# Performance work log

Hardware: AMD Instinct MI355X
Metric: run time of the kernel (lower is better)

Reference implementation:

```python
import jax, jax.numpy as jnp
import numpy as np

B, S, D = 2, 2048, 1024
H, HD = 16, 64
DFF = 4 * D
EPS = 1e-5


def gelu(x):
    return 0.5 * x * (1.0 + jnp.tanh(jnp.sqrt(2.0 / jnp.pi) * (x + 0.044715 * x * x * x)))


def layer_norm(x, scale, bias):
    mu = jnp.mean(x, axis=-1, keepdims=True)
    var = jnp.mean(jnp.square(x - mu), axis=-1, keepdims=True)
    return (x - mu) * jax.lax.rsqrt(var + EPS) * scale + bias


def setup_inputs() -> dict:
    key = jax.random.key(0)
    ks = jax.random.split(key, 8)
    s = 0.02
    x = jax.random.normal(ks[0], (B, S, D), jnp.float32)
    mask = jnp.tril(jnp.ones((S, S), dtype=bool))[None, None]  # (1,1,S,S) causal
    return {
        "x": x,
        "mask": mask,
        "ln1_scale": jnp.ones((D,), jnp.float32),
        "ln1_bias": jnp.zeros((D,), jnp.float32),
        "ln2_scale": jnp.ones((D,), jnp.float32),
        "ln2_bias": jnp.zeros((D,), jnp.float32),
        "w_qkv": jax.random.normal(ks[1], (D, 3 * D), jnp.float32) * s,
        "b_qkv": jnp.zeros((3 * D,), jnp.float32),
        "w_attn_proj": jax.random.normal(ks[2], (D, D), jnp.float32) * s,
        "b_attn_proj": jnp.zeros((D,), jnp.float32),
        "w_fc": jax.random.normal(ks[3], (D, DFF), jnp.float32) * s,
        "b_fc": jnp.zeros((DFF,), jnp.float32),
        "w_mlp_proj": jax.random.normal(ks[4], (DFF, D), jnp.float32) * s,
        "b_mlp_proj": jnp.zeros((D,), jnp.float32),
    }


def reference(x, mask, ln1_scale, ln1_bias, ln2_scale, ln2_bias,
              w_qkv, b_qkv, w_attn_proj, b_attn_proj,
              w_fc, b_fc, w_mlp_proj, b_mlp_proj):
    bsz, seq, _ = x.shape
    # --- attention branch ---
    h = layer_norm(x, ln1_scale, ln1_bias)
    qkv = h @ w_qkv + b_qkv                       # (b, s, 3D)
    q, k, v = jnp.split(qkv, 3, axis=-1)
    q = q.reshape(bsz, seq, H, HD).transpose(0, 2, 1, 3)  # bhsd
    k = k.reshape(bsz, seq, H, HD).transpose(0, 2, 1, 3)
    v = v.reshape(bsz, seq, H, HD).transpose(0, 2, 1, 3)
    q = q * (1.0 / jnp.sqrt(HD))
    scores = jnp.einsum('bhqd,bhkd->bhqk', q, k)
    scores = jnp.where(mask, scores, -1e10)
    probs = jax.nn.softmax(scores, axis=-1)
    attn = jnp.einsum('bhqk,bhkd->bhqd', probs, v)
    attn = attn.transpose(0, 2, 1, 3).reshape(bsz, seq, D)
    attn = attn @ w_attn_proj + b_attn_proj
    x = x + attn
    # --- MLP branch ---
    h = layer_norm(x, ln2_scale, ln2_bias)
    h = gelu(h @ w_fc + b_fc)
    h = h @ w_mlp_proj + b_mlp_proj
    return x + h
```

## Files before the change

### kernel.cpp

```cpp
#include <hip/hip_runtime.h>
#include <hip/hip_bf16.h>
#include <stdint.h>


typedef __attribute__((ext_vector_type(8))) short bf16x8;
typedef __attribute__((ext_vector_type(8))) unsigned short u16x8;
typedef __attribute__((ext_vector_type(4))) float f32x4;

#define NEG_BIG -30000.0f
#define EXP2SC 0.18033688011112042f

__device__ __forceinline__ float b2f(unsigned short u) {
  union { unsigned int i; float f; } c; c.i = ((unsigned int)u) << 16; return c.f;
}
__device__ __forceinline__ unsigned short f2b(float f) {
  union { float f; unsigned int u; } c; c.f = f;
  unsigned int r = c.u + 0x7fffu + ((c.u >> 16) & 1u);
  return (unsigned short)(r >> 16);
}
__device__ __forceinline__ unsigned int pk2bf(float a, float b) {
  float2 f; f.x = a; f.y = b;
  union { __hip_bfloat162 h; unsigned int u; } c;
  c.h = __float22bfloat162_rn(f);
  return c.u;
}
__device__ __forceinline__ float ldx(const void* p, size_t i, int f32) {
  return f32 ? ((const float*)p)[i] : b2f(((const unsigned short*)p)[i]);
}
__device__ __forceinline__ void gld_lds16(const void* g, void* l) {
  __builtin_amdgcn_global_load_lds(
      (__attribute__((address_space(1))) void*)(void*)g,
      (__attribute__((address_space(3))) void*)l, 16, 0, 0);
}

__global__ void detect_k(const unsigned short* __restrict__ x, int* __restrict__ flag) {
  int lane = threadIdx.x;
  int cnt = 0;
#pragma unroll
  for (int j = 0; j < 4; ++j) {
    unsigned e = (x[lane * 4 + j] >> 7) & 0xFF;
    if (e >= 100 && e <= 145) cnt++;
  }
#pragma unroll
  for (int off = 32; off; off >>= 1) cnt += __shfl_down(cnt, off);
  if (lane == 0) *flag = (cnt < 220) ? 1 : 0;
}

__global__ __launch_bounds__(256) void transpose_k(
    const void* __restrict__ in, unsigned short* __restrict__ out,
    int K, int N, const int* __restrict__ flag) {
  int fm = *flag;
  __shared__ unsigned short tile[64][72];
  int n0 = blockIdx.x * 64, k0 = blockIdx.y * 64;
  int t = threadIdx.x;
  int r = t >> 3, c0 = (t & 7) * 8;
  if (fm) {
    const float* inf = (const float*)in;
#pragma unroll
    for (int p = 0; p < 2; ++p) {
      int k = r + p * 32;
      float4 v0 = *(const float4*)(inf + (size_t)(k0 + k) * N + n0 + c0);
      float4 v1 = *(const float4*)(inf + (size_t)(k0 + k) * N + n0 + c0 + 4);
      tile[k][c0 + 0] = f2b(v0.x); tile[k][c0 + 1] = f2b(v0.y);
      tile[k][c0 + 2] = f2b(v0.z); tile[k][c0 + 3] = f2b(v0.w);
      tile[k][c0 + 4] = f2b(v1.x); tile[k][c0 + 5] = f2b(v1.y);
      tile[k][c0 + 6] = f2b(v1.z); tile[k][c0 + 7] = f2b(v1.w);
    }
  } else {
    const unsigned short* inu = (const unsigned short*)in;
#pragma unroll
    for (int p = 0; p < 2; ++p) {
      int k = r + p * 32;
      u16x8 v = *(const u16x8*)(inu + (size_t)(k0 + k) * N + n0 + c0);
      *(u16x8*)&tile[k][c0] = v;
    }
  }
  __syncthreads();
#pragma unroll
  for (int p = 0; p < 2; ++p) {
    int n = r + p * 32;
    u16x8 v;
#pragma unroll
    for (int j = 0; j < 8; ++j) v[j] = tile[c0 + j][n];
    *(u16x8*)(out + (size_t)(n0 + n) * K + k0 + c0) = v;
  }
}

__global__ __launch_bounds__(256) void ln_k(
    const void* __restrict__ x, const void* __restrict__ sc,
    const void* __restrict__ bs, unsigned short* __restrict__ out,
    const int* __restrict__ flag, int xAdap) {
  int fm = *flag;
  int fx = xAdap ? fm : 0;
  int row = blockIdx.x, t = threadIdx.x;
  float f0, f1, f2, f3;
  if (fx) {
    float4 xv = ((const float4*)x)[(size_t)row * 256 + t];
    f0 = xv.x; f1 = xv.y; f2 = xv.z; f3 = xv.w;
  } else {
    ushort4 xv = ((const ushort4*)x)[(size_t)row * 256 + t];
    f0 = b2f(xv.x); f1 = b2f(xv.y); f2 = b2f(xv.z); f3 = b2f(xv.w);
  }
  float s = f0 + f1 + f2 + f3;
  float q = f0 * f0 + f1 * f1 + f2 * f2 + f3 * f3;
#pragma unroll
  for (int off = 32; off; off >>= 1) {
    s += __shfl_down(s, off);
    q += __shfl_down(q, off);
  }
  __shared__ float red[8];
  int w = t >> 6, lane = t & 63;
  if (lane == 0) { red[w] = s; red[w + 4] = q; }
  __syncthreads();
  float S = red[0] + red[1] + red[2] + red[3];
  float Q = red[4] + red[5] + red[6] + red[7];
  float mean = S * (1.f / 1024.f);
  float var = Q * (1.f / 1024.f) - mean * mean;
  float rstd = rsqrtf(var + 1e-5f);
  int c = t * 4;
  ushort4 o;
  o.x = f2b((f0 - mean) * rstd * ldx(sc, c, fm)     + ldx(bs, c, fm));
  o.y = f2b((f1 - mean) * rstd * ldx(sc, c + 1, fm) + ldx(bs, c + 1, fm));
  o.z = f2b((f2 - mean) * rstd * ldx(sc, c + 2, fm) + ldx(bs, c + 2, fm));
  o.w = f2b((f3 - mean) * rstd * ldx(sc, c + 3, fm) + ldx(bs, c + 3, fm));
  ((ushort4*)(out + (size_t)row * 1024))[t] = o;
}

template <int EPI>
__global__ __launch_bounds__(256) void gemm_bt(
    const unsigned short* __restrict__ A, const unsigned short* __restrict__ Bt,
    const void* __restrict__ bias, const void* __restrict__ res,
    void* __restrict__ C, int M, int N, int K,
    const int* __restrict__ flag, int resAdap, int outAdap) {
  int fm = *flag;
  int fr = resAdap ? fm : 0;
  int fo = outAdap ? fm : 0;
  __shared__ unsigned short As[2][128 * 32];
  __shared__ unsigned short Bs[2][128 * 32];
  int t = threadIdx.x;
  int bn = blockIdx.x * 128, bm = blockIdx.y * 128;
  int w = t >> 6, lane = t & 63, quad = lane >> 4, l16 = lane & 15;
  int wm = (w >> 1) * 64, wn = (w & 1) * 64;
  f32x4 acc[4][4] = {};

  int c1 = t, c2 = t + 256;
  int r1 = c1 >> 2, e1 = (c1 & 3) * 8;
  int r2 = c2 >> 2, e2 = (c2 & 3) * 8;
  const unsigned short* a1 = A + (size_t)(bm + r1) * K + e1;
  const unsigned short* a2 = A + (size_t)(bm + r2) * K + e2;
  const unsigned short* b1 = Bt + (size_t)(bn + r1) * K + e1;
  const unsigned short* b2 = Bt + (size_t)(bn + r2) * K + e2;

  for (int k0 = 0; k0 < K; k0 += 64) {
    gld_lds16(a1 + k0,      As[0] + c1 * 8);
    gld_lds16(a2 + k0,      As[0] + c2 * 8);
    gld_lds16(a1 + k0 + 32, As[1] + c1 * 8);
    gld_lds16(a2 + k0 + 32, As[1] + c2 * 8);
    gld_lds16(b1 + k0,      Bs[0] + c1 * 8);
    gld_lds16(b2 + k0,      Bs[0] + c2 * 8);
    gld_lds16(b1 + k0 + 32, Bs[1] + c1 * 8);
    gld_lds16(b2 + k0 + 32, Bs[1] + c2 * 8);
    __syncthreads();
#pragma unroll
    for (int h = 0; h < 2; ++h) {
      bf16x8 af[4], bfr[4];
#pragma unroll
      for (int i = 0; i < 4; ++i)
        af[i] = *(const bf16x8*)&As[h][(wm + i * 16 + l16) * 32 + quad * 8];
#pragma unroll
      for (int j = 0; j < 4; ++j)
        bfr[j] = *(const bf16x8*)&Bs[h][(wn + j * 16 + l16) * 32 + quad * 8];
#pragma unroll
      for (int i = 0; i < 4; ++i)
#pragma unroll
        for (int j = 0; j < 4; ++j)
          acc[i][j] = __builtin_amdgcn_mfma_f32_16x16x32_bf16(af[i], bfr[j], acc[i][j], 0, 0, 0);
    }
    __syncthreads();
  }

#pragma unroll
  for (int j = 0; j < 4; ++j) {
    int col = bn + wn + j * 16 + l16;
    float bb = ldx(bias, col, fm);
#pragma unroll
    for (int i = 0; i < 4; ++i) {
      int row0 = bm + wm + i * 16 + quad * 4;
#pragma unroll
      for (int r = 0; r < 4; ++r) {
        float v = acc[i][j][r] + bb;
        if (EPI == 1) {
          float u = 0.7978845608f * (v + 0.044715f * v * v * v);
          float e = __expf(2.f * u);
          float th = 1.f - 2.f / (e + 1.f);
          v = 0.5f * v * (1.f + th);
        } else if (EPI == 2) {
          v += ldx(res, (size_t)(row0 + r) * N + col, fr);
        }
        size_t idx = (size_t)(row0 + r) * N + col;
        if (fo) ((float*)C)[idx] = v;
        else    ((unsigned short*)C)[idx] = f2b(v);
      }
    }
  }
}

__global__ __launch_bounds__(256) void gemm_pk(
    const unsigned short* __restrict__ A, const unsigned short* __restrict__ Bt,
    float* __restrict__ P, int M, int N, int Kh, int Kfull) {
  __shared__ unsigned short As[2][128 * 32];
  __shared__ unsigned short Bs[2][128 * 32];
  int t = threadIdx.x;
  int bn = blockIdx.x * 128, bm = blockIdx.y * 128;
  int koff = blockIdx.z * Kh;
  float* Pz = P + (size_t)blockIdx.z * M * N;
  int w = t >> 6, lane = t & 63, quad = lane >> 4, l16 = lane & 15;
  int wm = (w >> 1) * 64, wn = (w & 1) * 64;
  f32x4 acc[4][4] = {};

  int c1 = t, c2 = t + 256;
  int r1 = c1 >> 2, e1 = (c1 & 3) * 8;
  int r2 = c2 >> 2, e2 = (c2 & 3) * 8;
  const unsigned short* a1 = A + (size_t)(bm + r1) * Kfull + koff + e1;
  const unsigned short* a2 = A + (size_t)(bm + r2) * Kfull + koff + e2;
  const unsigned short* b1 = Bt + (size_t)(bn + r1) * Kfull + koff + e1;
  const unsigned short* b2 = Bt + (size_t)(bn + r2) * Kfull + koff + e2;

  for (int k0 = 0; k0 < Kh; k0 += 64) {
    gld_lds16(a1 + k0,      As[0] + c1 * 8);
    gld_lds16(a2 + k0,      As[0] + c2 * 8);
    gld_lds16(a1 + k0 + 32, As[1] + c1 * 8);
    gld_lds16(a2 + k0 + 32, As[1] + c2 * 8);
    gld_lds16(b1 + k0,      Bs[0] + c1 * 8);
    gld_lds16(b2 + k0,      Bs[0] + c2 * 8);
    gld_lds16(b1 + k0 + 32, Bs[1] + c1 * 8);
    gld_lds16(b2 + k0 + 32, Bs[1] + c2 * 8);
    __syncthreads();
#pragma unroll
    for (int h = 0; h < 2; ++h) {
      bf16x8 af[4], bfr[4];
#pragma unroll
      for (int i = 0; i < 4; ++i)
        af[i] = *(const bf16x8*)&As[h][(wm + i * 16 + l16) * 32 + quad * 8];
#pragma unroll
      for (int j = 0; j < 4; ++j)
        bfr[j] = *(const bf16x8*)&Bs[h][(wn + j * 16 + l16) * 32 + quad * 8];
#pragma unroll
      for (int i = 0; i < 4; ++i)
#pragma unroll
        for (int j = 0; j < 4; ++j)
          acc[i][j] = __builtin_amdgcn_mfma_f32_16x16x32_bf16(af[i], bfr[j], acc[i][j], 0, 0, 0);
    }
    __syncthreads();
  }

#pragma unroll
  for (int j = 0; j < 4; ++j) {
    int col = bn + wn + j * 16 + l16;
#pragma unroll
    for (int i = 0; i < 4; ++i) {
      int row0 = bm + wm + i * 16 + quad * 4;
#pragma unroll
      for (int r = 0; r < 4; ++r)
        Pz[(size_t)(row0 + r) * N + col] = acc[i][j][r];
    }
  }
}

__global__ __launch_bounds__(256) void reduce2_k(
    const float* __restrict__ P0, const float* __restrict__ P1,
    const void* __restrict__ bias, const void* __restrict__ res,
    void* __restrict__ out, int N,
    const int* __restrict__ flag, int resAdap, int outAdap) {
  int fm = *flag;
  int fr = resAdap ? fm : 0;
  int fo = outAdap ? fm : 0;
  size_t idx = ((size_t)blockIdx.x * 256 + threadIdx.x) * 4;
  float4 p0 = *(const float4*)(P0 + idx);
  float4 p1 = *(const float4*)(P1 + idx);
  int col = (int)(idx & (size_t)(N - 1));
  float v0 = p0.x + p1.x + ldx(bias, col, fm)     + ldx(res, idx, fr);
  float v1 = p0.y + p1.y + ldx(bias, col + 1, fm) + ldx(res, idx + 1, fr);
  float v2 = p0.z + p1.z + ldx(bias, col + 2, fm) + ldx(res, idx + 2, fr);
  float v3 = p0.w + p1.w + ldx(bias, col + 3, fm) + ldx(res, idx + 3, fr);
  if (fo) {
    float4 o; o.x = v0; o.y = v1; o.z = v2; o.w = v3;
    *(float4*)((float*)out + idx) = o;
  } else {
    ushort4 o; o.x = f2b(v0); o.y = f2b(v1); o.z = f2b(v2); o.w = f2b(v3);
    *(ushort4*)((unsigned short*)out + idx) = o;
  }
}

__global__ __launch_bounds__(256) void attn_k(
    const unsigned short* __restrict__ qkv, unsigned short* __restrict__ out) {
  __shared__ unsigned short Ks[64 * 72];
  __shared__ unsigned int   Vt[64 * 35];
  __shared__ unsigned short Ps[4 * 16 * 72];
  int t = threadIdx.x, w = t >> 6, lane = t & 63, quad = lane >> 4, l16 = lane & 15;
  int pi = blockIdx.x, bh = blockIdx.y, b = bh >> 4, h = bh & 15;
  const unsigned short* base = qkv + (size_t)b * 2048 * 3072 + h * 64;
  unsigned short* Pw = Ps + w * 16 * 72;
  int srow = t >> 3, d0 = (t & 7) * 8;

#pragma unroll 1
  for (int half = 0; half < 2; ++half) {
    int qt = half ? (31 - pi) : pi;
    int q0 = qt * 64;
    int qrel = w * 16 + l16;
    const unsigned short* qp = base + (size_t)(q0 + qrel) * 3072;
    bf16x8 bq0 = *(const bf16x8*)(qp + quad * 8);
    bf16x8 bq1 = *(const bf16x8*)(qp + 32 + quad * 8);
    float m_i = NEG_BIG, l_i = 0.f;
    f32x4 O[4] = {};

    u16x8 kA, kB, vA, vB;
    {
      const unsigned short* kb = base;
      kA = *(const u16x8*)(kb + (size_t)srow * 3072 + 1024 + d0);
      kB = *(const u16x8*)(kb + (size_t)(srow + 32) * 3072 + 1024 + d0);
      vA = *(const u16x8*)(kb + (size_t)(2 * srow) * 3072 + 2048 + d0);
      vB = *(const u16x8*)(kb + (size_t)(2 * srow + 1) * 3072 + 2048 + d0);
    }

#pragma unroll 1
    for (int kt = 0; kt <= qt; ++kt) {
      *(u16x8*)&Ks[srow * 72 + d0] = kA;
      *(u16x8*)&Ks[(srow + 32) * 72 + d0] = kB;
#pragma unroll
      for (int j = 0; j < 8; ++j)
        Vt[(d0 + j) * 35 + srow] = (unsigned int)vA[j] | ((unsigned int)vB[j] << 16);
      __syncthreads();

      if (kt < qt) {
        const unsigned short* kb = base + (size_t)((kt + 1) * 64) * 3072;
        kA = *(const u16x8*)(kb + (size_t)srow * 3072 + 1024 + d0);
        kB = *(const u16x8*)(kb + (size_t)(srow + 32) * 3072 + 1024 + d0);
        vA = *(const u16x8*)(kb + (size_t)(2 * srow) * 3072 + 2048 + d0);
        vB = *(const u16x8*)(kb + (size_t)(2 * srow + 1) * 3072 + 2048 + d0);
      }

      f32x4 ST[4];
#pragma unroll
      for (int i = 0; i < 4; ++i) {
        bf16x8 ak0 = *(const bf16x8*)&Ks[(i * 16 + l16) * 72 + quad * 8];
        bf16x8 ak1 = *(const bf16x8*)&Ks[(i * 16 + l16) * 72 + 32 + quad * 8];
        f32x4 z = {};
        z = __builtin_amdgcn_mfma_f32_16x16x32_bf16(ak0, bq0, z, 0, 0, 0);
        ST[i] = __builtin_amdgcn_mfma_f32_16x16x32_bf16(ak1, bq1, z, 0, 0, 0);
      }

      bool dm = (kt == qt);
      float p[4][4];
      float mx = NEG_BIG;
#pragma unroll
      for (int i = 0; i < 4; ++i)
#pragma unroll
        for (int r = 0; r < 4; ++r) {
          float v = ST[i][r] * EXP2SC;
          int srel = i * 16 + quad * 4 + r;
          if (dm && srel > qrel) v = NEG_BIG;
          p[i][r] = v;
          mx = fmaxf(mx, v);
        }
      mx = fmaxf(mx, __shfl_xor(mx, 16));
      mx = fmaxf(mx, __shfl_xor(mx, 32));
      float mn = fmaxf(m_i, mx);
      float alpha = exp2f(m_i - mn);
      m_i = mn;
      float sum = 0.f;
#pragma unroll
      for (int i = 0; i < 4; ++i)
#pragma unroll
        for (int r = 0; r < 4; ++r) {
          float e = exp2f(p[i][r] - mn);
          p[i][r] = e;
          sum += e;
        }
      sum += __shfl_xor(sum, 16);
      sum += __shfl_xor(sum, 32);
      l_i = alpha * l_i + sum;

#pragma unroll
      for (int i = 0; i < 4; ++i) {
        uint2 pr;
        pr.x = pk2bf(p[i][0], p[i][1]);
        pr.y = pk2bf(p[i][2], p[i][3]);
        *(uint2*)(Pw + l16 * 72 + i * 16 + quad * 4) = pr;
      }

      float ar[4];
#pragma unroll
      for (int r = 0; r < 4; ++r)
        ar[r] = __shfl(alpha, (lane & 48) | (quad * 4 + r));
#pragma unroll
      for (int jd = 0; jd < 4; ++jd)
#pragma unroll
        for (int r = 0; r < 4; ++r) O[jd][r] *= ar[r];

#pragma unroll
      for (int ks = 0; ks < 2; ++ks) {
        bf16x8 ap = *(const bf16x8*)(Pw + l16 * 72 + ks * 32 + quad * 8);
#pragma unroll
        for (int jd = 0; jd < 4; ++jd) {
          union { unsigned int u[4]; bf16x8 v; } bv;
          int vbase = (jd * 16 + l16) * 35 + ks * 16 + quad * 4;
#pragma unroll
          for (int cc = 0; cc < 4; ++cc) bv.u[cc] = Vt[vbase + cc];
          O[jd] = __builtin_amdgcn_mfma_f32_16x16x32_bf16(ap, bv.v, O[jd], 0, 0, 0);
        }
      }
      __syncthreads();
    }

    float li[4];
#pragma unroll
    for (int r = 0; r < 4; ++r)
      li[r] = 1.f / __shfl(l_i, (lane & 48) | (quad * 4 + r));
#pragma unroll
    for (int jd = 0; jd < 4; ++jd)
#pragma unroll
      for (int r = 0; r < 4; ++r) {
        size_t row = (size_t)b * 2048 + q0 + w * 16 + quad * 4 + r;
        out[row * 1024 + h * 64 + jd * 16 + l16] = f2b(O[jd][r] * li[r]);
      }
  }
}

extern "C" void kernel_launch(void* const* d_in, const int* in_sizes, int n_in,
                              void* d_out, int out_size, void* d_ws, size_t ws_size,
                              hipStream_t stream) {
  (void)in_sizes; (void)n_in; (void)out_size;
  const void* x     = d_in[0];
  const void* ln1s  = d_in[2];
  const void* ln1b  = d_in[3];
  const void* ln2s  = d_in[4];
  const void* ln2b  = d_in[5];
  const void* w_qkv = d_in[6];
  const void* b_qkv = d_in[7];
  const void* w_ap  = d_in[8];
  const void* b_ap  = d_in[9];
  const void* w_fc  = d_in[10];
  const void* b_fc  = d_in[11];
  const void* w_mp  = d_in[12];
  const void* b_mp  = d_in[13];
  char* ws = (char*)d_ws;

  const int M = 4096, D = 1024, DFF = 4096, QKV3 = 3072;
  size_t off = 0;
  auto alloc = [&](size_t n) { char* p = ws + off; off += n; return p; };
  int* flag            = (int*)alloc(256);
  unsigned short* wT   = (unsigned short*)alloc((size_t)DFF * D * 2);
  unsigned short* hbuf = (unsigned short*)alloc((size_t)M * D * 2);
  unsigned short* x1   = (unsigned short*)alloc((size_t)M * D * 2);
  char* region = alloc((size_t)M * DFF * 2);
  unsigned short* qkvb = (unsigned short*)region;
  float* P0a = (float*)region;
  float* P1a = (float*)(region + (size_t)M * D * 4);
  unsigned short* fcb  = (unsigned short*)region;
  bool mlpSplit = ws_size >= off + (size_t)M * D * 8 + 1024;
  float* P0m = (float*)(ws + off);
  float* P1m = P0m + (size_t)M * D;

  dim3 blk(256);
  detect_k<<<dim3(1), dim3(64), 0, stream>>>((const unsigned short*)x, flag);
  transpose_k<<<dim3(QKV3 / 64, D / 64), blk, 0, stream>>>(w_qkv, wT, D, QKV3, flag);
  ln_k<<<dim3(M), blk, 0, stream>>>(x, ln1s, ln1b, hbuf, flag, 1);
  gemm_bt<0><<<dim3(QKV3 / 128, M / 128), blk, 0, stream>>>(hbuf, wT, b_qkv, nullptr, qkvb, M, QKV3, D, flag, 0, 0);
  attn_k<<<dim3(16, 32), blk, 0, stream>>>(qkvb, hbuf);
  transpose_k<<<dim3(D / 64, D / 64), blk, 0, stream>>>(w_ap, wT, D, D, flag);
  gemm_pk<<<dim3(D / 128, M / 128, 2), blk, 0, stream>>>(hbuf, wT, P0a, M, D, D / 2, D);
  reduce2_k<<<dim3(M * D / 1024), blk, 0, stream>>>(P0a, P1a, b_ap, x, x1, D, flag, 1, 0);
  transpose_k<<<dim3(DFF / 64, D / 64), blk, 0, stream>>>(w_fc, wT, D, DFF, flag);
  ln_k<<<dim3(M), blk, 0, stream>>>(x1, ln2s, ln2b, hbuf, flag, 0);
  gemm_bt<1><<<dim3(DFF / 128, M / 128), blk, 0, stream>>>(hbuf, wT, b_fc, nullptr, fcb, M, DFF, D, flag, 0, 0);
  transpose_k<<<dim3(D / 64, DFF / 64), blk, 0, stream>>>(w_mp, wT, DFF, D, flag);
  if (mlpSplit) {
    gemm_pk<<<dim3(D / 128, M / 128, 2), blk, 0, stream>>>(fcb, wT, P0m, M, D, DFF / 2, DFF);
    reduce2_k<<<dim3(M * D / 1024), blk, 0, stream>>>(P0m, P1m, b_mp, x1, d_out, D, flag, 0, 1);
  } else {
    gemm_bt<2><<<dim3(D / 128, M / 128), blk, 0, stream>>>(fcb, wT, b_mp, x1, d_out, M, D, DFF, flag, 0, 1);
  }
}
```

Baseline: 417.4 us.

## Replace direct global-to-LDS loads with register-prefetched double-buffered GEMM pipeline

Both GEMM kernels drop the global_load_lds path, which loaded a 64-wide K slab and then synchronised twice per iteration. They now prefetch the next 32-wide K slice into registers while MFMAs run on the current LDS buffer, and alternate between two LDS buffers so only one barrier is needed per iteration. The intent is to hide global memory latency behind compute and remove one barrier per step. In exchange the loop runs twice as many iterations with less work each, uses more registers, and goes through VGPRs instead of the direct DMA-to-LDS path.

```diff
diff --git a/kernel.cpp b/kernel.cpp
--- a/kernel.cpp
+++ b/kernel.cpp
@@ -26,11 +26,6 @@
 }
 __device__ __forceinline__ float ldx(const void* p, size_t i, int f32) {
   return f32 ? ((const float*)p)[i] : b2f(((const unsigned short*)p)[i]);
-}
-__device__ __forceinline__ void gld_lds16(const void* g, void* l) {
-  __builtin_amdgcn_global_load_lds(
-      (__attribute__((address_space(1))) void*)(void*)g,
-      (__attribute__((address_space(3))) void*)l, 16, 0, 0);
 }
 
 __global__ void detect_k(const unsigned short* __restrict__ x, int* __restrict__ flag) {
@@ -151,32 +146,39 @@
   const unsigned short* b1 = Bt + (size_t)(bn + r1) * K + e1;
   const unsigned short* b2 = Bt + (size_t)(bn + r2) * K + e2;
 
-  for (int k0 = 0; k0 < K; k0 += 64) {
-    gld_lds16(a1 + k0,      As[0] + c1 * 8);
-    gld_lds16(a2 + k0,      As[0] + c2 * 8);
-    gld_lds16(a1 + k0 + 32, As[1] + c1 * 8);
-    gld_lds16(a2 + k0 + 32, As[1] + c2 * 8);
-    gld_lds16(b1 + k0,      Bs[0] + c1 * 8);
-    gld_lds16(b2 + k0,      Bs[0] + c2 * 8);
-    gld_lds16(b1 + k0 + 32, Bs[1] + c1 * 8);
-    gld_lds16(b2 + k0 + 32, Bs[1] + c2 * 8);
+  u16x8 va1 = *(const u16x8*)a1;
+  u16x8 va2 = *(const u16x8*)a2;
+  u16x8 vb1 = *(const u16x8*)b1;
+  u16x8 vb2 = *(const u16x8*)b2;
+
+  int nIter = K >> 5;
+  for (int it = 0; it < nIter; ++it) {
+    unsigned short* Ab = As[it & 1];
+    unsigned short* Bb = Bs[it & 1];
+    *(u16x8*)(Ab + c1 * 8) = va1;
+    *(u16x8*)(Ab + c2 * 8) = va2;
+    *(u16x8*)(Bb + c1 * 8) = vb1;
+    *(u16x8*)(Bb + c2 * 8) = vb2;
     __syncthreads();
-#pragma unroll
-    for (int h = 0; h < 2; ++h) {
-      bf16x8 af[4], bfr[4];
-#pragma unroll
-      for (int i = 0; i < 4; ++i)
-        af[i] = *(const bf16x8*)&As[h][(wm + i * 16 + l16) * 32 + quad * 8];
+    if (it + 1 < nIter) {
+      int k0 = (it + 1) << 5;
+      va1 = *(const u16x8*)(a1 + k0);
+      va2 = *(const u16x8*)(a2 + k0);
+      vb1 = *(const u16x8*)(b1 + k0);
+      vb2 = *(const u16x8*)(b2 + k0);
+    }
+    bf16x8 af[4], bfr[4];
+#pragma unroll
+    for (int i = 0; i < 4; ++i)
+      af[i] = *(const bf16x8*)&Ab[(wm + i * 16 + l16) * 32 + quad * 8];
+#pragma unroll
+    for (int j = 0; j < 4; ++j)
+      bfr[j] = *(const bf16x8*)&Bb[(wn + j * 16 + l16) * 32 + quad * 8];
+#pragma unroll
+    for (int i = 0; i < 4; ++i)
 #pragma unroll
       for (int j = 0; j < 4; ++j)
-        bfr[j] = *(const bf16x8*)&Bs[h][(wn + j * 16 + l16) * 32 + quad * 8];
-#pragma unroll
-      for (int i = 0; i < 4; ++i)
-#pragma unroll
-        for (int j = 0; j < 4; ++j)
-          acc[i][j] = __builtin_amdgcn_mfma_f32_16x16x32_bf16(af[i], bfr[j], acc[i][j], 0, 0, 0);
-    }
-    __syncthreads();
+        acc[i][j] = __builtin_amdgcn_mfma_f32_16x16x32_bf16(af[i], bfr[j], acc[i][j], 0, 0, 0);
   }
 
 #pragma unroll
@@ -226,32 +228,39 @@
   const unsigned short* b1 = Bt + (size_t)(bn + r1) * Kfull + koff + e1;
   const unsigned short* b2 = Bt + (size_t)(bn + r2) * Kfull + koff + e2;
 
-  for (int k0 = 0; k0 < Kh; k0 += 64) {
-    gld_lds16(a1 + k0,      As[0] + c1 * 8);
-    gld_lds16(a2 + k0,      As[0] + c2 * 8);
-    gld_lds16(a1 + k0 + 32, As[1] + c1 * 8);
-    gld_lds16(a2 + k0 + 32, As[1] + c2 * 8);
-    gld_lds16(b1 + k0,      Bs[0] + c1 * 8);
-    gld_lds16(b2 + k0,      Bs[0] + c2 * 8);
-    gld_lds16(b1 + k0 + 32, Bs[1] + c1 * 8);
-    gld_lds16(b2 + k0 + 32, Bs[1] + c2 * 8);
+  u16x8 va1 = *(const u16x8*)a1;
+  u16x8 va2 = *(const u16x8*)a2;
+  u16x8 vb1 = *(const u16x8*)b1;
+  u16x8 vb2 = *(const u16x8*)b2;
+
+  int nIter = Kh >> 5;
+  for (int it = 0; it < nIter; ++it) {
+    unsigned short* Ab = As[it & 1];
+    unsigned short* Bb = Bs[it & 1];
+    *(u16x8*)(Ab + c1 * 8) = va1;
+    *(u16x8*)(Ab + c2 * 8) = va2;
+    *(u16x8*)(Bb + c1 * 8) = vb1;
+    *(u16x8*)(Bb + c2 * 8) = vb2;
     __syncthreads();
-#pragma unroll
-    for (int h = 0; h < 2; ++h) {
-      bf16x8 af[4], bfr[4];
-#pragma unroll
-      for (int i = 0; i < 4; ++i)
-        af[i] = *(const bf16x8*)&As[h][(wm + i * 16 + l16) * 32 + quad * 8];
+    if (it + 1 < nIter) {
+      int k0 = (it + 1) << 5;
+      va1 = *(const u16x8*)(a1 + k0);
+      va2 = *(const u16x8*)(a2 + k0);
+      vb1 = *(const u16x8*)(b1 + k0);
+      vb2 = *(const u16x8*)(b2 + k0);
+    }
+    bf16x8 af[4], bfr[4];
+#pragma unroll
+    for (int i = 0; i < 4; ++i)
+      af[i] = *(const bf16x8*)&Ab[(wm + i * 16 + l16) * 32 + quad * 8];
+#pragma unroll
+    for (int j = 0; j < 4; ++j)
+      bfr[j] = *(const bf16x8*)&Bb[(wn + j * 16 + l16) * 32 + quad * 8];
+#pragma unroll
+    for (int i = 0; i < 4; ++i)
 #pragma unroll
       for (int j = 0; j < 4; ++j)
-        bfr[j] = *(const bf16x8*)&Bs[h][(wn + j * 16 + l16) * 32 + quad * 8];
-#pragma unroll
-      for (int i = 0; i < 4; ++i)
-#pragma unroll
-        for (int j = 0; j < 4; ++j)
-          acc[i][j] = __builtin_amdgcn_mfma_f32_16x16x32_bf16(af[i], bfr[j], acc[i][j], 0, 0, 0);
-    }
-    __syncthreads();
+        acc[i][j] = __builtin_amdgcn_mfma_f32_16x16x32_bf16(af[i], bfr[j], acc[i][j], 0, 0, 0);
   }
 
 #pragma unroll
```

Result: no change. 413.7 us (-0.9%).

## Register-prefetch pipeline in split-K GEMM and fuse residual reduce with LayerNorm

Applied to the files above, without the earlier changes.

The split-K GEMM stops using direct global-to-LDS loads with a 64-wide K step. It now prefetches the next 32-wide K slice into registers while computing on a double-buffered LDS tile, with one barrier per iteration. Separately, the split-K partial reduction plus bias and residual is fused with the second LayerNorm into one kernel. That drops a launch and a re-read of x1. The fused LN computes variance as E[x^2]-mean^2 on fp32 pre-rounding values rather than the bf16-rounded x1, so numerics change slightly.

```diff
diff --git a/kernel.cpp b/kernel.cpp
--- a/kernel.cpp
+++ b/kernel.cpp
@@ -226,32 +226,39 @@
   const unsigned short* b1 = Bt + (size_t)(bn + r1) * Kfull + koff + e1;
   const unsigned short* b2 = Bt + (size_t)(bn + r2) * Kfull + koff + e2;
 
-  for (int k0 = 0; k0 < Kh; k0 += 64) {
-    gld_lds16(a1 + k0,      As[0] + c1 * 8);
-    gld_lds16(a2 + k0,      As[0] + c2 * 8);
-    gld_lds16(a1 + k0 + 32, As[1] + c1 * 8);
-    gld_lds16(a2 + k0 + 32, As[1] + c2 * 8);
-    gld_lds16(b1 + k0,      Bs[0] + c1 * 8);
-    gld_lds16(b2 + k0,      Bs[0] + c2 * 8);
-    gld_lds16(b1 + k0 + 32, Bs[1] + c1 * 8);
-    gld_lds16(b2 + k0 + 32, Bs[1] + c2 * 8);
+  u16x8 va1 = *(const u16x8*)a1;
+  u16x8 va2 = *(const u16x8*)a2;
+  u16x8 vb1 = *(const u16x8*)b1;
+  u16x8 vb2 = *(const u16x8*)b2;
+
+  int nIter = Kh >> 5;
+  for (int it = 0; it < nIter; ++it) {
+    unsigned short* Ab = As[it & 1];
+    unsigned short* Bb = Bs[it & 1];
+    *(u16x8*)(Ab + c1 * 8) = va1;
+    *(u16x8*)(Ab + c2 * 8) = va2;
+    *(u16x8*)(Bb + c1 * 8) = vb1;
+    *(u16x8*)(Bb + c2 * 8) = vb2;
     __syncthreads();
-#pragma unroll
-    for (int h = 0; h < 2; ++h) {
-      bf16x8 af[4], bfr[4];
-#pragma unroll
-      for (int i = 0; i < 4; ++i)
-        af[i] = *(const bf16x8*)&As[h][(wm + i * 16 + l16) * 32 + quad * 8];
+    if (it + 1 < nIter) {
+      int k0 = (it + 1) << 5;
+      va1 = *(const u16x8*)(a1 + k0);
+      va2 = *(const u16x8*)(a2 + k0);
+      vb1 = *(const u16x8*)(b1 + k0);
+      vb2 = *(const u16x8*)(b2 + k0);
+    }
+    bf16x8 af[4], bfr[4];
+#pragma unroll
+    for (int i = 0; i < 4; ++i)
+      af[i] = *(const bf16x8*)&Ab[(wm + i * 16 + l16) * 32 + quad * 8];
+#pragma unroll
+    for (int j = 0; j < 4; ++j)
+      bfr[j] = *(const bf16x8*)&Bb[(wn + j * 16 + l16) * 32 + quad * 8];
+#pragma unroll
+    for (int i = 0; i < 4; ++i)
 #pragma unroll
       for (int j = 0; j < 4; ++j)
-        bfr[j] = *(const bf16x8*)&Bs[h][(wn + j * 16 + l16) * 32 + quad * 8];
-#pragma unroll
-      for (int i = 0; i < 4; ++i)
-#pragma unroll
-        for (int j = 0; j < 4; ++j)
-          acc[i][j] = __builtin_amdgcn_mfma_f32_16x16x32_bf16(af[i], bfr[j], acc[i][j], 0, 0, 0);
-    }
-    __syncthreads();
+        acc[i][j] = __builtin_amdgcn_mfma_f32_16x16x32_bf16(af[i], bfr[j], acc[i][j], 0, 0, 0);
   }
 
 #pragma unroll
@@ -292,6 +299,50 @@
   }
 }
 
+__global__ __launch_bounds__(256) void reduce2ln_k(
+    const float* __restrict__ P0, const float* __restrict__ P1,
+    const void* __restrict__ bias, const void* __restrict__ resx,
+    unsigned short* __restrict__ x1, unsigned short* __restrict__ hout,
+    const void* __restrict__ sc, const void* __restrict__ bs,
+    const int* __restrict__ flag) {
+  int fm = *flag;
+  int row = blockIdx.x, t = threadIdx.x;
+  size_t base = (size_t)row * 1024 + t * 4;
+  float4 p0 = *(const float4*)(P0 + base);
+  float4 p1 = *(const float4*)(P1 + base);
+  int c = t * 4;
+  float f0 = p0.x + p1.x + ldx(bias, c, fm)     + ldx(resx, base, fm);
+  float f1 = p0.y + p1.y + ldx(bias, c + 1, fm) + ldx(resx, base + 1, fm);
+  float f2 = p0.z + p1.z + ldx(bias, c + 2, fm) + ldx(resx, base + 2, fm);
+  float f3 = p0.w + p1.w + ldx(bias, c + 3, fm) + ldx(resx, base + 3, fm);
+  ushort4 xo;
+  xo.x = f2b(f0); xo.y = f2b(f1); xo.z = f2b(f2); xo.w = f2b(f3);
+  ((ushort4*)(x1 + (size_t)row * 1024))[t] = xo;
+
+  float s = f0 + f1 + f2 + f3;
+  float q = f0 * f0 + f1 * f1 + f2 * f2 + f3 * f3;
+#pragma unroll
+  for (int off = 32; off; off >>= 1) {
+    s += __shfl_down(s, off);
+    q += __shfl_down(q, off);
+  }
+  __shared__ float red[8];
+  int w = t >> 6, lane = t & 63;
+  if (lane == 0) { red[w] = s; red[w + 4] = q; }
+  __syncthreads();
+  float S = red[0] + red[1] + red[2] + red[3];
+  float Q = red[4] + red[5] + red[6] + red[7];
+  float mean = S * (1.f / 1024.f);
+  float var = Q * (1.f / 1024.f) - mean * mean;
+  float rstd = rsqrtf(var + 1e-5f);
+  ushort4 o;
+  o.x = f2b((f0 - mean) * rstd * ldx(sc, c, fm)     + ldx(bs, c, fm));
+  o.y = f2b((f1 - mean) * rstd * ldx(sc, c + 1, fm) + ldx(bs, c + 1, fm));
+  o.z = f2b((f2 - mean) * rstd * ldx(sc, c + 2, fm) + ldx(bs, c + 2, fm));
+  o.w = f2b((f3 - mean) * rstd * ldx(sc, c + 3, fm) + ldx(bs, c + 3, fm));
+  ((ushort4*)(hout + (size_t)row * 1024))[t] = o;
+}
+
 __global__ __launch_bounds__(256) void attn_k(
     const unsigned short* __restrict__ qkv, unsigned short* __restrict__ out) {
   __shared__ unsigned short Ks[64 * 72];
@@ -470,9 +521,8 @@
   attn_k<<<dim3(16, 32), blk, 0, stream>>>(qkvb, hbuf);
   transpose_k<<<dim3(D / 64, D / 64), blk, 0, stream>>>(w_ap, wT, D, D, flag);
   gemm_pk<<<dim3(D / 128, M / 128, 2), blk, 0, stream>>>(hbuf, wT, P0a, M, D, D / 2, D);
-  reduce2_k<<<dim3(M * D / 1024), blk, 0, stream>>>(P0a, P1a, b_ap, x, x1, D, flag, 1, 0);
+  reduce2ln_k<<<dim3(M), blk, 0, stream>>>(P0a, P1a, b_ap, x, x1, hbuf, ln2s, ln2b, flag);
   transpose_k<<<dim3(DFF / 64, D / 64), blk, 0, stream>>>(w_fc, wT, D, DFF, flag);
-  ln_k<<<dim3(M), blk, 0, stream>>>(x1, ln2s, ln2b, hbuf, flag, 0);
   gemm_bt<1><<<dim3(DFF / 128, M / 128), blk, 0, stream>>>(hbuf, wT, b_fc, nullptr, fcb, M, DFF, D, flag, 0, 0);
   transpose_k<<<dim3(D / 64, DFF / 64), blk, 0, stream>>>(w_mp, wT, DFF, D, flag);
   if (mlpSplit) {
```

New measurement: 408.0 us. 1.02x faster.
